# Kernel tuning notes

Measured on AMD Instinct MI355X. Metric: run time of the kernel, lower is better.

The kernel has to match this reference:

```python
import jax, jax.numpy as jnp
import numpy as np

N_HEADS = 16

def setup_inputs() -> dict:
    key = jax.random.key(0)
    ks = jax.random.split(key, 8)
    B, S, D = 2, 2048, 2048
    H, hd = N_HEADS, D // N_HEADS
    w_scale = 0.02  # keep pre-softmax logits in a sane range
    return {
        "x": jax.random.normal(ks[0], (B, S, D), jnp.float32),
        "Wq": jax.random.normal(ks[1], (D, D), jnp.float32) * w_scale,
        "bq": jax.random.normal(ks[2], (D,), jnp.float32) * w_scale,
        "Wk": jax.random.normal(ks[3], (D, D), jnp.float32) * w_scale,
        "bk": jax.random.normal(ks[4], (D,), jnp.float32) * w_scale,
        "Wv": jax.random.normal(ks[5], (D, D), jnp.float32) * w_scale,
        "bv": jax.random.normal(ks[6], (D,), jnp.float32) * w_scale,
        "k_cache": jnp.zeros((B, H, S, hd), jnp.float32),
        "v_cache": jnp.zeros((B, H, S, hd), jnp.float32),
        "start_pos": 0,
    }

def reference(x, Wq, bq, Wk, bk, Wv, bv, k_cache, v_cache, start_pos):
    B, S, D = x.shape
    H = N_HEADS
    hd = D // H
    # qkv projections (nn.Linear equivalent)
    q_val = (x @ Wq + bq).reshape(B, H, S, hd)  # faithful .view: pure reshape, NO transpose
    k_val = (x @ Wk + bk).reshape(B, H, S, hd)
    v_val = (x @ Wv + bv).reshape(B, H, S, hd)
    # KV-cache scatter update at input_pos = [start_pos, start_pos+S)
    pos = jnp.arange(S) + start_pos
    k_cache = k_cache.at[:, :, pos].set(k_val)
    v_cache = v_cache.at[:, :, pos].set(v_val)
    L = k_cache.shape[2]
    # QK^T / sqrt(hd)
    scores = jnp.einsum('bhsd,bhld->bhsl', q_val, k_cache) / jnp.sqrt(jnp.asarray(hd, x.dtype))
    # default mask path: triu(ones, diag=1) is the KEEP mask (faithful to source)
    mask = jnp.triu(jnp.ones((S, L), x.dtype), 1)
    scores = scores - 1e9 * (1.0 - mask)
    probs = jax.nn.softmax(scores, axis=-1)
    out = jnp.einsum('bhsl,bhld->bhsd', probs, v_cache)  # [B,H,S,hd]
    return out.reshape(B, S, D)  # faithful .view(B, -1, D)
```

## Files before the change

### kernel.cpp

```cpp
#include <hip/hip_runtime.h>
#include <math.h>

#define BATCH 2
#define SEQ   2048
#define DIM   2048
#define NH    16
#define HD    128
#define MTOT  (BATCH*SEQ)
static constexpr float SCALE  = 0.08838834764831845f;
static constexpr float L2E    = 1.4426950408889634f;
static constexpr float QSCALE = SCALE * L2E;
static constexpr float MASKC  = 1.0e9f * L2E;


typedef short s8  __attribute__((ext_vector_type(8)));
typedef float f4  __attribute__((ext_vector_type(4)));

__device__ inline unsigned short bf_rn(float f) {
    union { float f; unsigned u; } v; v.f = f;
    unsigned r = v.u + 0x7FFFu + ((v.u >> 16) & 1u);
    return (unsigned short)(r >> 16);
}

#define GLL(g, l) __builtin_amdgcn_global_load_lds( \
    (const __attribute__((address_space(1))) void*)(g), \
    (__attribute__((address_space(3))) void*)(l), 16, 0, 0)

__global__ __launch_bounds__(256) void convert_x(
    const float* __restrict__ x, unsigned short* __restrict__ xh)
{
    size_t i = ((size_t)blockIdx.x * 256 + threadIdx.x) * 4;
    float4 v = *(const float4*)(x + i);
    float a[4] = {v.x, v.y, v.z, v.w};
    ushort4 h;
    unsigned short* hp = &h.x;
    #pragma unroll
    for (int j = 0; j < 4; ++j) hp[j] = bf_rn(a[j]);
    *(ushort4*)(xh + i) = h;
}

__global__ __launch_bounds__(256) void convert_wT(
    const float* __restrict__ Wq, const float* __restrict__ Wk,
    const float* __restrict__ Wv,
    unsigned short* __restrict__ Wth)
{
    const int z = blockIdx.z;
    const float* W = (z == 0) ? Wq : (z == 1) ? Wk : Wv;
    unsigned short* th = Wth + (size_t)z * DIM * DIM;

    __shared__ unsigned short Th[64][72];

    const int k0 = blockIdx.x * 64;
    const int n0 = blockIdx.y * 64;
    const int tid = threadIdx.x;

    #pragma unroll
    for (int i = 0; i < 4; ++i) {
        int idx = tid + i * 256;
        int kk = idx >> 4, n4 = idx & 15;
        float4 w = *(const float4*)(W + (size_t)(k0 + kk) * DIM + n0 + n4 * 4);
        float a[4] = {w.x, w.y, w.z, w.w};
        #pragma unroll
        for (int j = 0; j < 4; ++j)
            Th[n4 * 4 + j][kk] = bf_rn(a[j]);
    }
    __syncthreads();
    #pragma unroll
    for (int i = 0; i < 2; ++i) {
        int idx = tid + i * 256;
        int nn = idx >> 3, c = idx & 7;
        *(uint4*)(th + (size_t)(n0 + nn) * DIM + k0 + c * 8) =
            *(const uint4*)(&Th[nn][c * 8]);
    }
}

__global__ __launch_bounds__(256) void qkv_mfma_split(
    const unsigned short* __restrict__ xh,
    const unsigned short* __restrict__ Wth,
    const float* __restrict__ bq, const float* __restrict__ bk,
    const float* __restrict__ bv,
    unsigned short* __restrict__ qh_, unsigned short* __restrict__ kh_,
    unsigned short* __restrict__ vh_)
{
    const int z = blockIdx.z;
    const unsigned short* Bhg = Wth + (size_t)z * DIM * DIM;
    const float* bias = (z == 0) ? bq : (z == 1) ? bk : bv;
    unsigned short* dh = (z == 0) ? qh_ : (z == 1) ? kh_ : vh_;
    const float oscale = (z == 0) ? QSCALE : 1.0f;

    const int bm = blockIdx.x * 128;
    const int bn = blockIdx.y * 128;

    __shared__ unsigned short Ah[128 * 32];
    __shared__ unsigned short Bh[128 * 32];

    const int tid = threadIdx.x;
    const int w = tid >> 6, lane = tid & 63;
    const int wr = w >> 1, wc = w & 1;
    const int lr = lane & 15, lg = lane >> 4;

    const int rA0 = bm + (2 * w + 0) * 16 + (lane >> 2);
    const int rA1 = bm + (2 * w + 1) * 16 + (lane >> 2);
    const int rB0 = bn + (2 * w + 0) * 16 + (lane >> 2);
    const int rB1 = bn + (2 * w + 1) * 16 + (lane >> 2);
    const int kin = (lane & 3) * 8;
    const unsigned short* gah0 = xh + (size_t)rA0 * DIM + kin;
    const unsigned short* gah1 = xh + (size_t)rA1 * DIM + kin;
    const unsigned short* gbh0 = Bhg + (size_t)rB0 * DIM + kin;
    const unsigned short* gbh1 = Bhg + (size_t)rB1 * DIM + kin;
    unsigned short* lah0 = &Ah[(2 * w + 0) * 512];
    unsigned short* lah1 = &Ah[(2 * w + 1) * 512];
    unsigned short* lbh0 = &Bh[(2 * w + 0) * 512];
    unsigned short* lbh1 = &Bh[(2 * w + 1) * 512];

    f4 zero4 = {0.f, 0.f, 0.f, 0.f};
    f4 acc[4][4];
    #pragma unroll
    for (int mi = 0; mi < 4; ++mi)
        #pragma unroll
        for (int ni = 0; ni < 4; ++ni) acc[mi][ni] = zero4;

    const unsigned short* pAh = &Ah[(wr * 64 + lr) * 32 + lg * 8];
    const unsigned short* pBh = &Bh[(wc * 64 + lr) * 32 + lg * 8];

    for (int k0 = 0; k0 < DIM; k0 += 32) {
        GLL(gah0 + k0, lah0); GLL(gah1 + k0, lah1);
        GLL(gbh0 + k0, lbh0); GLL(gbh1 + k0, lbh1);
        __syncthreads();

        s8 fah[4], fbh[4];
        #pragma unroll
        for (int i = 0; i < 4; ++i) {
            fah[i] = *(const s8*)(pAh + i * 512);
            fbh[i] = *(const s8*)(pBh + i * 512);
        }
        #pragma unroll
        for (int mi = 0; mi < 4; ++mi)
            #pragma unroll
            for (int ni = 0; ni < 4; ++ni)
                acc[mi][ni] = __builtin_amdgcn_mfma_f32_16x16x32_bf16(
                    fah[mi], fbh[ni], acc[mi][ni], 0, 0, 0);
        __syncthreads();
    }

    float bv_[4]; int col_[4];
    #pragma unroll
    for (int ni = 0; ni < 4; ++ni) {
        col_[ni] = bn + wc * 64 + ni * 16 + lr;
        bv_[ni] = bias[col_[ni]];
    }
    #pragma unroll
    for (int mi = 0; mi < 4; ++mi)
        #pragma unroll
        for (int ni = 0; ni < 4; ++ni)
            #pragma unroll
            for (int r = 0; r < 4; ++r) {
                int row = bm + wr * 64 + mi * 16 + lg * 4 + r;
                float v = (acc[mi][ni][r] + bv_[ni]) * oscale;
                dh[(size_t)row * DIM + col_[ni]] = bf_rn(v);
            }
}

__global__ __launch_bounds__(256) void transpose_v(
    const unsigned short* __restrict__ vh, unsigned short* __restrict__ vth)
{
    __shared__ unsigned short T[64][72];
    const int s0 = blockIdx.x * 64;
    const int d0 = blockIdx.y * 64;
    const int bh = blockIdx.z;
    const int tid = threadIdx.x;
    {
        const int r = tid >> 2, cs = tid & 3;
        size_t g = ((size_t)bh * SEQ + s0 + r) * HD + d0 + cs * 16;
        *(uint4*)(&T[r][cs * 16])     = *(const uint4*)(vh + g);
        *(uint4*)(&T[r][cs * 16 + 8]) = *(const uint4*)(vh + g + 8);
    }
    __syncthreads();
    {
        const int d = tid >> 2, ss = tid & 3;
        unsigned short bh_[16];
        #pragma unroll
        for (int j = 0; j < 16; ++j)
            bh_[j] = T[ss * 16 + j][d];
        size_t t = ((size_t)bh * HD + d0 + d) * SEQ + s0 + ss * 16;
        *(uint4*)(vth + t)     = ((const uint4*)bh_)[0];
        *(uint4*)(vth + t + 8) = ((const uint4*)bh_)[1];
    }
}

#define KVBLK 32
#define NT    (SEQ / KVBLK)
#define PSTR  40

__global__ __launch_bounds__(256) void attn_mfma(
    const unsigned short* __restrict__ qh,
    const unsigned short* __restrict__ kh,
    const unsigned short* __restrict__ vth,
    float* __restrict__ out)
{
    __shared__ unsigned short KhA[KVBLK * HD], KhB[KVBLK * HD];
    __shared__ unsigned short VhA[HD * KVBLK], VhB[HD * KVBLK];
    __shared__ unsigned short Ph[4][32 * PSTR];

    const int bid  = blockIdx.x;
    const int slot = bid >> 8;
    const int idx  = bid & 255;
    const int bh_i = idx >> 3;
    const int j    = idx & 7;
    const int qb   = slot ? (14 - j)
                          : (j == 0 ? 0 : (j == 1 ? 15 : j - 1));
    const int h  = bh_i & 15;
    const int b  = bh_i >> 4;
    const int qs = qb * 128;

    const int tid = threadIdx.x;
    const int w = tid >> 6, lane = tid & 63;
    const int lr = lane & 15, lg = lane >> 4;
    const int q0 = w * 32;

    const size_t hbase = (size_t)(b * NH + h) * SEQ * HD;

    s8 fqh[2][4];
    #pragma unroll
    for (int mi = 0; mi < 2; ++mi)
        #pragma unroll
        for (int k4 = 0; k4 < 4; ++k4) {
            size_t off = hbase + (size_t)(qs + q0 + mi * 16 + lr) * HD
                       + (size_t)((k4 * 4 + lg) * 8);
            fqh[mi][k4] = *(const s8*)(qh + off);
        }

    s8 ones;
    #pragma unroll
    for (int i = 0; i < 8; ++i) ones[i] = (short)0x3F80;

    f4 O[2][8], Os[2];
    f4 zero4 = {0.f, 0.f, 0.f, 0.f};
    #pragma unroll
    for (int mi = 0; mi < 2; ++mi) {
        #pragma unroll
        for (int nj = 0; nj < 8; ++nj) O[mi][nj] = zero4;
        Os[mi] = zero4;
    }
    float mrun[2][4];
    #pragma unroll
    for (int mi = 0; mi < 2; ++mi)
        #pragma unroll
        for (int r = 0; r < 4; ++r) mrun[mi][r] = -INFINITY;

    const int kr0 = (2 * w + 0) * 4 + (lane >> 4);
    const int kr1 = (2 * w + 1) * 4 + (lane >> 4);
    const int ks  = lane & 15;
    const int vd0 = (2 * w + 0) * 16 + (lane >> 2);
    const int vd1 = (2 * w + 1) * 16 + (lane >> 2);
    const int vs  = lane & 3;
    const size_t kg0 = hbase + (size_t)kr0 * HD + (size_t)((ks ^ (kr0 & 7)) * 8);
    const size_t kg1 = hbase + (size_t)kr1 * HD + (size_t)((ks ^ (kr1 & 7)) * 8);
    const size_t vg0 = hbase + (size_t)vd0 * SEQ + (size_t)((vs ^ (vd0 & 3)) * 8);
    const size_t vg1 = hbase + (size_t)vd1 * SEQ + (size_t)((vs ^ (vd1 & 3)) * 8);

    const int t0 = (qb == 15) ? 0 : qb * 4;

#define STAGE(T_, KH_, VH_) do {                                             \
        const size_t koff = (size_t)(T_) * KVBLK * HD;                       \
        const int    loff = (T_) * KVBLK;                                    \
        GLL(kh + kg0 + koff, &KH_[(2 * w + 0) * 512]);                       \
        GLL(kh + kg1 + koff, &KH_[(2 * w + 1) * 512]);                       \
        GLL(vth + vg0 + loff, &VH_[(2 * w + 0) * 512]);                      \
        GLL(vth + vg1 + loff, &VH_[(2 * w + 1) * 512]);                      \
    } while (0)

    auto compute = [&](int t, const unsigned short* KH, const unsigned short* VH) {
        const int l0 = t * KVBLK;

        s8 fkh[2][4];
        #pragma unroll
        for (int nj = 0; nj < 2; ++nj) {
            const int n = nj * 16 + lr;
            #pragma unroll
            for (int k4 = 0; k4 < 4; ++k4) {
                const int sl = (k4 * 4 + lg) ^ (n & 7);
                fkh[nj][k4] = *(const s8*)(&KH[n * HD + sl * 8]);
            }
        }
        f4 sc[2][2];
        #pragma unroll
        for (int mi = 0; mi < 2; ++mi)
            #pragma unroll
            for (int nj = 0; nj < 2; ++nj) sc[mi][nj] = zero4;
        #pragma unroll
        for (int k4 = 0; k4 < 4; ++k4)
            #pragma unroll
            for (int mi = 0; mi < 2; ++mi)
                #pragma unroll
                for (int nj = 0; nj < 2; ++nj)
                    sc[mi][nj] = __builtin_amdgcn_mfma_f32_16x16x32_bf16(
                        fqh[mi][k4], fkh[nj][k4], sc[mi][nj], 0, 0, 0);

        float v0[2][4], v1[2][4];
        bool need = false;
        #pragma unroll
        for (int mi = 0; mi < 2; ++mi)
            #pragma unroll
            for (int r = 0; r < 4; ++r) {
                const int srow = qs + q0 + mi * 16 + lg * 4 + r;
                float a = sc[mi][0][r];
                float c = sc[mi][1][r];
                if (l0 + lr      <= srow) a -= MASKC;
                if (l0 + 16 + lr <= srow) c -= MASKC;
                v0[mi][r] = a; v1[mi][r] = c;
                const float lim = mrun[mi][r] + 11.5f;
                need = need || (a > lim) || (c > lim);
            }

        if (__any(need)) {
            #pragma unroll
            for (int mi = 0; mi < 2; ++mi)
                #pragma unroll
                for (int r = 0; r < 4; ++r) {
                    float rmax = fmaxf(v0[mi][r], v1[mi][r]);
                    #pragma unroll
                    for (int m_ = 1; m_ < 16; m_ <<= 1)
                        rmax = fmaxf(rmax, __shfl_xor(rmax, m_, 64));
                    const float mnew = fmaxf(mrun[mi][r], rmax);
                    const float corr = exp2f(mrun[mi][r] - mnew);
                    mrun[mi][r] = mnew;
                    #pragma unroll
                    for (int nj = 0; nj < 8; ++nj) O[mi][nj][r] *= corr;
                    Os[mi][r] *= corr;
                }
        }

        #pragma unroll
        for (int mi = 0; mi < 2; ++mi)
            #pragma unroll
            for (int r = 0; r < 4; ++r) {
                const float p0 = exp2f(v0[mi][r] - mrun[mi][r]);
                const float p1 = exp2f(v1[mi][r] - mrun[mi][r]);
                const int q = mi * 16 + lg * 4 + r;
                Ph[w][q * PSTR + lr]      = bf_rn(p0);
                Ph[w][q * PSTR + 16 + lr] = bf_rn(p1);
            }

        s8 fph[2], fvh[8];
        #pragma unroll
        for (int mi = 0; mi < 2; ++mi)
            fph[mi] = *(const s8*)(&Ph[w][(mi * 16 + lr) * PSTR + lg * 8]);
        #pragma unroll
        for (int nj = 0; nj < 8; ++nj) {
            const int d = nj * 16 + lr;
            const int sl = lg ^ (d & 3);
            fvh[nj] = *(const s8*)(&VH[d * KVBLK + sl * 8]);
        }
        #pragma unroll
        for (int mi = 0; mi < 2; ++mi) {
            #pragma unroll
            for (int nj = 0; nj < 8; ++nj)
                O[mi][nj] = __builtin_amdgcn_mfma_f32_16x16x32_bf16(
                    fph[mi], fvh[nj], O[mi][nj], 0, 0, 0);
            Os[mi] = __builtin_amdgcn_mfma_f32_16x16x32_bf16(
                fph[mi], ones, Os[mi], 0, 0, 0);
        }
    };

    STAGE(t0, KhA, VhA);
    __syncthreads();
    for (int t = t0; t < NT; t += 2) {
        STAGE(t + 1, KhB, VhB);
        compute(t, KhA, VhA);
        __syncthreads();
        if (t + 2 < NT) STAGE(t + 2, KhA, VhA);
        compute(t + 1, KhB, VhB);
        __syncthreads();
    }
#undef STAGE

    float* op = out + hbase;
    float inv[2][4];
    #pragma unroll
    for (int mi = 0; mi < 2; ++mi)
        #pragma unroll
        for (int r = 0; r < 4; ++r) inv[mi][r] = 1.f / Os[mi][r];
    #pragma unroll
    for (int mi = 0; mi < 2; ++mi)
        #pragma unroll
        for (int nj = 0; nj < 8; ++nj)
            #pragma unroll
            for (int r = 0; r < 4; ++r) {
                const int srow = qs + q0 + mi * 16 + lg * 4 + r;
                op[(size_t)srow * HD + nj * 16 + lr] = O[mi][nj][r] * inv[mi][r];
            }
}

__global__ __launch_bounds__(256) void qkv_gemm(
    const float* __restrict__ x,
    const float* __restrict__ Wq, const float* __restrict__ bq,
    const float* __restrict__ Wk, const float* __restrict__ bk,
    const float* __restrict__ Wv, const float* __restrict__ bv,
    float* __restrict__ Qo, float* __restrict__ Ko, float* __restrict__ Vo)
{
    const int z = blockIdx.z;
    const float* W    = (z == 0) ? Wq : (z == 1) ? Wk : Wv;
    const float* bias = (z == 0) ? bq : (z == 1) ? bk : bv;
    float*       dst  = (z == 0) ? Qo : (z == 1) ? Ko : Vo;

    __shared__ float As[32][64];
    __shared__ float Bs[32][64];

    const int row0 = blockIdx.x * 64;
    const int col0 = blockIdx.y * 64;
    const int tid  = threadIdx.x;
    const int tm   = tid >> 4;
    const int tn   = tid & 15;

    float acc[4][4] = {};

    for (int k0 = 0; k0 < DIM; k0 += 32) {
        #pragma unroll
        for (int i = 0; i < 2; ++i) {
            int f = tid + i * 256;
            int r = f >> 3, c4 = f & 7;
            float4 a = *(const float4*)(x + (size_t)(row0 + r) * DIM + k0 + c4 * 4);
            As[c4 * 4 + 0][r] = a.x;
            As[c4 * 4 + 1][r] = a.y;
            As[c4 * 4 + 2][r] = a.z;
            As[c4 * 4 + 3][r] = a.w;
        }
        #pragma unroll
        for (int i = 0; i < 2; ++i) {
            int f = tid + i * 256;
            int r = f >> 4, c4 = f & 15;
            *(float4*)(&Bs[r][c4 * 4]) =
                *(const float4*)(W + (size_t)(k0 + r) * DIM + col0 + c4 * 4);
        }
        __syncthreads();
        #pragma unroll
        for (int k = 0; k < 32; ++k) {
            float4 a4 = *(const float4*)(&As[k][tm * 4]);
            float4 b4 = *(const float4*)(&Bs[k][tn * 4]);
            float av[4] = {a4.x, a4.y, a4.z, a4.w};
            float bw[4] = {b4.x, b4.y, b4.z, b4.w};
            #pragma unroll
            for (int i = 0; i < 4; ++i)
                #pragma unroll
                for (int j2 = 0; j2 < 4; ++j2)
                    acc[i][j2] += av[i] * bw[j2];
        }
        __syncthreads();
    }

    float4 bb = *(const float4*)(bias + col0 + tn * 4);
    float bsv[4] = {bb.x, bb.y, bb.z, bb.w};
    #pragma unroll
    for (int i = 0; i < 4; ++i) {
        int r = row0 + tm * 4 + i;
        float4 o;
        o.x = acc[i][0] + bsv[0];
        o.y = acc[i][1] + bsv[1];
        o.z = acc[i][2] + bsv[2];
        o.w = acc[i][3] + bsv[3];
        *(float4*)(dst + (size_t)r * DIM + col0 + tn * 4) = o;
    }
}

__global__ __launch_bounds__(256) void attn_kernel(
    const float* Qbuf,
    const float* __restrict__ Kc,
    const float* __restrict__ Vc,
    float* Out)
{
    __shared__ float smem[16384];
    float* QsT = smem;
    float* Ks  = smem + 8192;
    float* Ps  = smem + 8192;

    const int bid = blockIdx.x;
    const int qb  = bid & 31;
    const int h   = (bid >> 5) & 15;
    const int b   = bid >> 9;
    const size_t base = (size_t)b * SEQ * DIM + (size_t)h * SEQ * HD;
    const float* Qp = Qbuf + base;
    const float* Kp = Kc + base;
    const float* Vp = Vc + base;
    float*       Op = Out + base;

    const int tid = threadIdx.x;
    const int tm  = tid >> 4;
    const int tn  = tid & 15;
    const int qs  = qb * 64;

    #pragma unroll
    for (int i = 0; i < 8; ++i) {
        int f = tid + i * 256;
        int r = f >> 5, c4 = f & 31;
        float4 q = *(const float4*)(Qp + (size_t)(qs + r) * HD + c4 * 4);
        QsT[(c4 * 4 + 0) * 64 + r] = q.x;
        QsT[(c4 * 4 + 1) * 64 + r] = q.y;
        QsT[(c4 * 4 + 2) * 64 + r] = q.z;
        QsT[(c4 * 4 + 3) * 64 + r] = q.w;
    }

    float O[4][8] = {};
    float mrun[4], lrun[4];
    #pragma unroll
    for (int i = 0; i < 4; ++i) { mrun[i] = -INFINITY; lrun[i] = 0.f; }

    const int t0 = (qb == 31) ? 0 : qb;

    __syncthreads();

    for (int t = t0; t < 32; ++t) {
        const int l0 = t * 64;

        #pragma unroll
        for (int i = 0; i < 8; ++i) {
            int f = tid + i * 256;
            int r = f >> 5, c4 = f & 31;
            float4 kv = *(const float4*)(Kp + (size_t)(l0 + r) * HD + c4 * 4);
            int sc4 = c4 ^ ((r >> 2) & 7);
            *(float4*)(&Ks[r * 128 + sc4 * 4]) = kv;
        }
        __syncthreads();

        float sc[4][4] = {};
        for (int k4 = 0; k4 < 32; ++k4) {
            const int kb = k4 * 4;
            float qv[4][4];
            #pragma unroll
            for (int kk = 0; kk < 4; ++kk) {
                float4 q = *(const float4*)(&QsT[(kb + kk) * 64 + tm * 4]);
                qv[kk][0] = q.x; qv[kk][1] = q.y; qv[kk][2] = q.z; qv[kk][3] = q.w;
            }
            float kvv[4][4];
            #pragma unroll
            for (int j = 0; j < 4; ++j) {
                const int n = tn * 4 + j;
                float4 kv = *(const float4*)(&Ks[n * 128 + ((k4 ^ (tn & 7)) << 2)]);
                kvv[j][0] = kv.x; kvv[j][1] = kv.y; kvv[j][2] = kv.z; kvv[j][3] = kv.w;
            }
            #pragma unroll
            for (int kk = 0; kk < 4; ++kk)
                #pragma unroll
                for (int i = 0; i < 4; ++i)
                    #pragma unroll
                    for (int j = 0; j < 4; ++j)
                        sc[i][j] += qv[kk][i] * kvv[j][kk];
        }

        #pragma unroll
        for (int i = 0; i < 4; ++i) {
            const int srow = qs + tm * 4 + i;
            #pragma unroll
            for (int j = 0; j < 4; ++j) {
                float v = sc[i][j] * SCALE;
                const int l = l0 + tn * 4 + j;
                if (l <= srow) v -= 1e9f;
                sc[i][j] = v;
            }
        }

        float corr[4], rsum[4];
        #pragma unroll
        for (int i = 0; i < 4; ++i) {
            float rmax = fmaxf(fmaxf(sc[i][0], sc[i][1]), fmaxf(sc[i][2], sc[i][3]));
            #pragma unroll
            for (int off = 1; off < 16; off <<= 1)
                rmax = fmaxf(rmax, __shfl_xor(rmax, off, 64));
            const float mnew = fmaxf(mrun[i], rmax);
            corr[i] = __expf(mrun[i] - mnew);
            mrun[i] = mnew;
            float s = 0.f;
            #pragma unroll
            for (int j = 0; j < 4; ++j) {
                const float p = __expf(sc[i][j] - mnew);
                sc[i][j] = p;
                s += p;
            }
            #pragma unroll
            for (int off = 1; off < 16; off <<= 1)
                s += __shfl_xor(s, off, 64);
            rsum[i] = s;
        }
        #pragma unroll
        for (int i = 0; i < 4; ++i) {
            lrun[i] = lrun[i] * corr[i] + rsum[i];
            #pragma unroll
            for (int d = 0; d < 8; ++d) O[i][d] *= corr[i];
        }

        __syncthreads();

        #pragma unroll
        for (int i = 0; i < 4; ++i) {
            float4 p4 = make_float4(sc[i][0], sc[i][1], sc[i][2], sc[i][3]);
            *(float4*)(&Ps[(tm * 4 + i) * 68 + tn * 4]) = p4;
        }
        __syncthreads();

        for (int n4 = 0; n4 < 16; ++n4) {
            float pa[4][4];
            #pragma unroll
            for (int i = 0; i < 4; ++i) {
                float4 p = *(const float4*)(&Ps[(tm * 4 + i) * 68 + n4 * 4]);
                pa[i][0] = p.x; pa[i][1] = p.y; pa[i][2] = p.z; pa[i][3] = p.w;
            }
            #pragma unroll
            for (int nn = 0; nn < 4; ++nn) {
                const int l = l0 + n4 * 4 + nn;
                const float4 v0 = *(const float4*)(Vp + (size_t)l * HD + tn * 8);
                const float4 v1 = *(const float4*)(Vp + (size_t)l * HD + tn * 8 + 4);
                #pragma unroll
                for (int i = 0; i < 4; ++i) {
                    const float p = pa[i][nn];
                    O[i][0] += p * v0.x; O[i][1] += p * v0.y;
                    O[i][2] += p * v0.z; O[i][3] += p * v0.w;
                    O[i][4] += p * v1.x; O[i][5] += p * v1.y;
                    O[i][6] += p * v1.z; O[i][7] += p * v1.w;
                }
            }
        }
        __syncthreads();
    }

    #pragma unroll
    for (int i = 0; i < 4; ++i) {
        const float inv = 1.f / lrun[i];
        const int r = qs + tm * 4 + i;
        float4 o0 = make_float4(O[i][0] * inv, O[i][1] * inv, O[i][2] * inv, O[i][3] * inv);
        float4 o1 = make_float4(O[i][4] * inv, O[i][5] * inv, O[i][6] * inv, O[i][7] * inv);
        *(float4*)(Op + (size_t)r * HD + tn * 8)     = o0;
        *(float4*)(Op + (size_t)r * HD + tn * 8 + 4) = o1;
    }
}

extern "C" void kernel_launch(void* const* d_in, const int* in_sizes, int n_in,
                              void* d_out, int out_size, void* d_ws, size_t ws_size,
                              hipStream_t stream) {
    const float* x  = (const float*)d_in[0];
    const float* Wq = (const float*)d_in[1];
    const float* bq = (const float*)d_in[2];
    const float* Wk = (const float*)d_in[3];
    const float* bk = (const float*)d_in[4];
    const float* Wv = (const float*)d_in[5];
    const float* bv = (const float*)d_in[6];

    float* out = (float*)d_out;

    const size_t NM = (size_t)MTOT * DIM;
    const size_t DD = (size_t)DIM * DIM;

    const size_t NEED2 = NM * 16 + DD * 6;

    if (ws_size >= NEED2) {
        unsigned short* xh  = (unsigned short*)d_ws;
        unsigned short* xl  = xh + NM;
        unsigned short* Wth = xl + NM;
        unsigned short* qh_ = Wth + 3 * DD;
        unsigned short* ql_ = qh_ + NM;
        unsigned short* kh_ = ql_ + NM;
        unsigned short* kl_ = kh_ + NM;
        unsigned short* vh_ = kl_ + NM;
        unsigned short* vth = xh;

        convert_x<<<dim3((unsigned)(NM / 4 / 256)), 256, 0, stream>>>(x, xh);
        convert_wT<<<dim3(32, 32, 3), 256, 0, stream>>>(Wq, Wk, Wv, Wth);
        qkv_mfma_split<<<dim3(MTOT / 128, DIM / 128, 3), 256, 0, stream>>>(
            xh, Wth, bq, bk, bv, qh_, kh_, vh_);
        transpose_v<<<dim3(SEQ / 64, HD / 64, BATCH * NH), 256, 0, stream>>>(
            vh_, vth);
        attn_mfma<<<dim3(BATCH * NH * (SEQ / 128)), 256, 0, stream>>>(
            qh_, kh_, vth, out);
    } else {
        float* Kbuf = (float*)d_ws;
        float* Vbuf = Kbuf + NM;
        qkv_gemm<<<dim3(MTOT / 64, DIM / 64, 3), 256, 0, stream>>>(
            x, Wq, bq, Wk, bk, Wv, bv, out, Kbuf, Vbuf);
        attn_kernel<<<dim3(BATCH * NH * (SEQ / 64)), 256, 0, stream>>>(
            out, Kbuf, Vbuf, out);
    }
}
```

Measured before the change: 264.9 us.

## Halve attention query tile to 64 rows per block and double grid size

The attention kernel now gives each wave 16 query rows instead of 32, so a block covers 64 query rows, and the grid doubles to 1024 blocks. The block ordering is changed to launch the longest query block (qb=31, full KV range) first, followed by the rest. A minimum-occupancy hint of 3 blocks per CU is added to launch_bounds. The aim is more blocks and fewer registers per wave for better occupancy and load balance, at the cost of loading each K/V tile twice as often per query row and doing less MFMA work per LDS load.

```diff
diff --git a/kernel.cpp b/kernel.cpp
--- a/kernel.cpp
+++ b/kernel.cpp
@@ -192,7 +192,7 @@
 #define NT    (SEQ / KVBLK)
 #define PSTR  40
 
-__global__ __launch_bounds__(256) void attn_mfma(
+__global__ __launch_bounds__(256, 3) void attn_mfma(
     const unsigned short* __restrict__ qh,
     const unsigned short* __restrict__ kh,
     const unsigned short* __restrict__ vth,
@@ -200,53 +200,43 @@
 {
     __shared__ unsigned short KhA[KVBLK * HD], KhB[KVBLK * HD];
     __shared__ unsigned short VhA[HD * KVBLK], VhB[HD * KVBLK];
-    __shared__ unsigned short Ph[4][32 * PSTR];
+    __shared__ unsigned short Ph[4][16 * PSTR];
 
     const int bid  = blockIdx.x;
-    const int slot = bid >> 8;
-    const int idx  = bid & 255;
-    const int bh_i = idx >> 3;
-    const int j    = idx & 7;
-    const int qb   = slot ? (14 - j)
-                          : (j == 0 ? 0 : (j == 1 ? 15 : j - 1));
-    const int h  = bh_i & 15;
-    const int b  = bh_i >> 4;
-    const int qs = qb * 128;
+    const int slot = bid >> 5;
+    const int bhi  = bid & 31;
+    const int qb   = (slot == 0) ? 31 : slot - 1;
+    const int h  = bhi & 15;
+    const int b  = bhi >> 4;
+    const int qs = qb * 64;
 
     const int tid = threadIdx.x;
     const int w = tid >> 6, lane = tid & 63;
     const int lr = lane & 15, lg = lane >> 4;
-    const int q0 = w * 32;
+    const int q0 = w * 16;
 
     const size_t hbase = (size_t)(b * NH + h) * SEQ * HD;
 
-    s8 fqh[2][4];
-    #pragma unroll
-    for (int mi = 0; mi < 2; ++mi)
-        #pragma unroll
-        for (int k4 = 0; k4 < 4; ++k4) {
-            size_t off = hbase + (size_t)(qs + q0 + mi * 16 + lr) * HD
-                       + (size_t)((k4 * 4 + lg) * 8);
-            fqh[mi][k4] = *(const s8*)(qh + off);
-        }
+    s8 fqh[4];
+    #pragma unroll
+    for (int k4 = 0; k4 < 4; ++k4) {
+        size_t off = hbase + (size_t)(qs + q0 + lr) * HD
+                   + (size_t)((k4 * 4 + lg) * 8);
+        fqh[k4] = *(const s8*)(qh + off);
+    }
 
     s8 ones;
     #pragma unroll
     for (int i = 0; i < 8; ++i) ones[i] = (short)0x3F80;
 
-    f4 O[2][8], Os[2];
+    f4 O[8], Os;
     f4 zero4 = {0.f, 0.f, 0.f, 0.f};
     #pragma unroll
-    for (int mi = 0; mi < 2; ++mi) {
-        #pragma unroll
-        for (int nj = 0; nj < 8; ++nj) O[mi][nj] = zero4;
-        Os[mi] = zero4;
-    }
-    float mrun[2][4];
-    #pragma unroll
-    for (int mi = 0; mi < 2; ++mi)
-        #pragma unroll
-        for (int r = 0; r < 4; ++r) mrun[mi][r] = -INFINITY;
+    for (int nj = 0; nj < 8; ++nj) O[nj] = zero4;
+    Os = zero4;
+    float mrun[4];
+    #pragma unroll
+    for (int r = 0; r < 4; ++r) mrun[r] = -INFINITY;
 
     const int kr0 = (2 * w + 0) * 4 + (lane >> 4);
     const int kr1 = (2 * w + 1) * 4 + (lane >> 4);
@@ -259,7 +249,7 @@
     const size_t vg0 = hbase + (size_t)vd0 * SEQ + (size_t)((vs ^ (vd0 & 3)) * 8);
     const size_t vg1 = hbase + (size_t)vd1 * SEQ + (size_t)((vs ^ (vd1 & 3)) * 8);
 
-    const int t0 = (qb == 15) ? 0 : qb * 4;
+    const int t0 = (qb == 31) ? 0 : qb * 2;
 
 #define STAGE(T_, KH_, VH_) do {                                             \
         const size_t koff = (size_t)(T_) * KVBLK * HD;                       \
@@ -283,69 +273,56 @@
                 fkh[nj][k4] = *(const s8*)(&KH[n * HD + sl * 8]);
             }
         }
-        f4 sc[2][2];
-        #pragma unroll
-        for (int mi = 0; mi < 2; ++mi)
-            #pragma unroll
-            for (int nj = 0; nj < 2; ++nj) sc[mi][nj] = zero4;
+        f4 sc[2];
+        sc[0] = zero4; sc[1] = zero4;
         #pragma unroll
         for (int k4 = 0; k4 < 4; ++k4)
             #pragma unroll
-            for (int mi = 0; mi < 2; ++mi)
+            for (int nj = 0; nj < 2; ++nj)
+                sc[nj] = __builtin_amdgcn_mfma_f32_16x16x32_bf16(
+                    fqh[k4], fkh[nj][k4], sc[nj], 0, 0, 0);
+
+        float v0[4], v1[4];
+        bool need = false;
+        #pragma unroll
+        for (int r = 0; r < 4; ++r) {
+            const int srow = qs + q0 + lg * 4 + r;
+            float a = sc[0][r];
+            float c = sc[1][r];
+            if (l0 + lr      <= srow) a -= MASKC;
+            if (l0 + 16 + lr <= srow) c -= MASKC;
+            v0[r] = a; v1[r] = c;
+            const float lim = mrun[r] + 11.5f;
+            need = need || (a > lim) || (c > lim);
+        }
+
+        if (__any(need)) {
+            #pragma unroll
+            for (int r = 0; r < 4; ++r) {
+                float rmax = fmaxf(v0[r], v1[r]);
                 #pragma unroll
-                for (int nj = 0; nj < 2; ++nj)
-                    sc[mi][nj] = __builtin_amdgcn_mfma_f32_16x16x32_bf16(
-                        fqh[mi][k4], fkh[nj][k4], sc[mi][nj], 0, 0, 0);
-
-        float v0[2][4], v1[2][4];
-        bool need = false;
-        #pragma unroll
-        for (int mi = 0; mi < 2; ++mi)
-            #pragma unroll
-            for (int r = 0; r < 4; ++r) {
-                const int srow = qs + q0 + mi * 16 + lg * 4 + r;
-                float a = sc[mi][0][r];
-                float c = sc[mi][1][r];
-                if (l0 + lr      <= srow) a -= MASKC;
-                if (l0 + 16 + lr <= srow) c -= MASKC;
-                v0[mi][r] = a; v1[mi][r] = c;
-                const float lim = mrun[mi][r] + 11.5f;
-                need = need || (a > lim) || (c > lim);
-            }
-
-        if (__any(need)) {
-            #pragma unroll
-            for (int mi = 0; mi < 2; ++mi)
+                for (int m_ = 1; m_ < 16; m_ <<= 1)
+                    rmax = fmaxf(rmax, __shfl_xor(rmax, m_, 64));
+                const float mnew = fmaxf(mrun[r], rmax);
+                const float corr = exp2f(mrun[r] - mnew);
+                mrun[r] = mnew;
                 #pragma unroll
-                for (int r = 0; r < 4; ++r) {
-                    float rmax = fmaxf(v0[mi][r], v1[mi][r]);
-                    #pragma unroll
-                    for (int m_ = 1; m_ < 16; m_ <<= 1)
-                        rmax = fmaxf(rmax, __shfl_xor(rmax, m_, 64));
-                    const float mnew = fmaxf(mrun[mi][r], rmax);
-                    const float corr = exp2f(mrun[mi][r] - mnew);
-                    mrun[mi][r] = mnew;
-                    #pragma unroll
-                    for (int nj = 0; nj < 8; ++nj) O[mi][nj][r] *= corr;
-                    Os[mi][r] *= corr;
-                }
-        }
-
-        #pragma unroll
-        for (int mi = 0; mi < 2; ++mi)
-            #pragma unroll
-            for (int r = 0; r < 4; ++r) {
-                const float p0 = exp2f(v0[mi][r] - mrun[mi][r]);
-                const float p1 = exp2f(v1[mi][r] - mrun[mi][r]);
-                const int q = mi * 16 + lg * 4 + r;
-                Ph[w][q * PSTR + lr]      = bf_rn(p0);
-                Ph[w][q * PSTR + 16 + lr] = bf_rn(p1);
-            }
-
-        s8 fph[2], fvh[8];
-        #pragma unroll
-        for (int mi = 0; mi < 2; ++mi)
-            fph[mi] = *(const s8*)(&Ph[w][(mi * 16 + lr) * PSTR + lg * 8]);
+                for (int nj = 0; nj < 8; ++nj) O[nj][r] *= corr;
+                Os[r] *= corr;
+            }
+        }
+
+        #pragma unroll
+        for (int r = 0; r < 4; ++r) {
+            const float p0 = exp2f(v0[r] - mrun[r]);
+            const float p1 = exp2f(v1[r] - mrun[r]);
+            const int q = lg * 4 + r;
+            Ph[w][q * PSTR + lr]      = bf_rn(p0);
+            Ph[w][q * PSTR + 16 + lr] = bf_rn(p1);
+        }
+
+        s8 fph, fvh[8];
+        fph = *(const s8*)(&Ph[w][lr * PSTR + lg * 8]);
         #pragma unroll
         for (int nj = 0; nj < 8; ++nj) {
             const int d = nj * 16 + lr;
@@ -353,14 +330,10 @@
             fvh[nj] = *(const s8*)(&VH[d * KVBLK + sl * 8]);
         }
         #pragma unroll
-        for (int mi = 0; mi < 2; ++mi) {
-            #pragma unroll
-            for (int nj = 0; nj < 8; ++nj)
-                O[mi][nj] = __builtin_amdgcn_mfma_f32_16x16x32_bf16(
-                    fph[mi], fvh[nj], O[mi][nj], 0, 0, 0);
-            Os[mi] = __builtin_amdgcn_mfma_f32_16x16x32_bf16(
-                fph[mi], ones, Os[mi], 0, 0, 0);
-        }
+        for (int nj = 0; nj < 8; ++nj)
+            O[nj] = __builtin_amdgcn_mfma_f32_16x16x32_bf16(
+                fph, fvh[nj], O[nj], 0, 0, 0);
+        Os = __builtin_amdgcn_mfma_f32_16x16x32_bf16(fph, ones, Os, 0, 0, 0);
     };
 
     STAGE(t0, KhA, VhA);
@@ -376,20 +349,16 @@
 #undef STAGE
 
     float* op = out + hbase;
-    float inv[2][4];
-    #pragma unroll
-    for (int mi = 0; mi < 2; ++mi)
-        #pragma unroll
-        for (int r = 0; r < 4; ++r) inv[mi][r] = 1.f / Os[mi][r];
-    #pragma unroll
-    for (int mi = 0; mi < 2; ++mi)
-        #pragma unroll
-        for (int nj = 0; nj < 8; ++nj)
-            #pragma unroll
-            for (int r = 0; r < 4; ++r) {
-                const int srow = qs + q0 + mi * 16 + lg * 4 + r;
-                op[(size_t)srow * HD + nj * 16 + lr] = O[mi][nj][r] * inv[mi][r];
-            }
+    float inv[4];
+    #pragma unroll
+    for (int r = 0; r < 4; ++r) inv[r] = 1.f / Os[r];
+    #pragma unroll
+    for (int nj = 0; nj < 8; ++nj)
+        #pragma unroll
+        for (int r = 0; r < 4; ++r) {
+            const int srow = qs + q0 + lg * 4 + r;
+            op[(size_t)srow * HD + nj * 16 + lr] = O[nj][r] * inv[r];
+        }
 }
 
 __global__ __launch_bounds__(256) void qkv_gemm(
@@ -668,7 +637,7 @@
             xh, Wth, bq, bk, bv, qh_, kh_, vh_);
         transpose_v<<<dim3(SEQ / 64, HD / 64, BATCH * NH), 256, 0, stream>>>(
             vh_, vth);
-        attn_mfma<<<dim3(BATCH * NH * (SEQ / 128)), 256, 0, stream>>>(
+        attn_mfma<<<dim3(BATCH * NH * (SEQ / 64)), 256, 0, stream>>>(
             qh_, kh_, vth, out);
     } else {
         float* Kbuf = (float*)d_ws;
```

Measured after the change: 218.8 us (median of 2 runs). -17.4%, faster.
